# Kernel tuning notes

Measured on AMD Instinct MI355X. Metric: run time of the kernel, lower is better.

The kernel has to match this reference:

```python
import jax, jax.numpy as jnp
import numpy as np

HEADS = 16
DV = 64  # value_out_channel
DK = 64  # key_out_channel == query_out_channel
DQ = 64  # query_out_channel


def setup_inputs() -> dict:
    key = jax.random.key(0)
    ks = jax.random.split(key, 7)
    B, Skv, Ekv = 4, 2048, 1024
    Sq, Eq = 2048, 1024
    x = jax.random.normal(ks[0], (B, Skv, Ekv), dtype=jnp.float32)
    y = jax.random.normal(ks[1], (B, Sq, Eq), dtype=jnp.float32)
    # Linear weights stored as [in, out] for x @ W; no bias on qkv (bias=False)
    Wv = jax.random.normal(ks[2], (Ekv, HEADS * DV), dtype=jnp.float32) * (Ekv ** -0.5)
    Wk = jax.random.normal(ks[3], (Ekv, HEADS * DK), dtype=jnp.float32) * (Ekv ** -0.5)
    Wq = jax.random.normal(ks[4], (Eq, HEADS * DQ), dtype=jnp.float32) * (Eq ** -0.5)
    Wu = jax.random.normal(ks[5], (HEADS * DV, DQ), dtype=jnp.float32) * ((HEADS * DV) ** -0.5)
    bu = jax.random.normal(ks[6], (DQ,), dtype=jnp.float32) * 0.01
    return {"x": x, "y": y, "Wv": Wv, "Wk": Wk, "Wq": Wq, "Wu": Wu, "bu": bu}


def reference(x, y, Wv, Wk, Wq, Wu, bu):
    B, Skv, Ekv = x.shape
    _, Sq, Eq = y.shape
    v = (x @ Wv).reshape(B, Skv, HEADS, DV)
    k = (x @ Wk).reshape(B, Skv, HEADS, DK)
    q = (y @ Wq).reshape(B, Sq, HEADS, DQ)
    # scaling uses INPUT embedding dims, as in the source
    q = q * (Eq ** -0.25)
    k = k * (Ekv ** -0.25)
    dot = jnp.einsum("bqhd,bkhd->bhqk", q, k)  # [B, H, Sq, Skv]
    attn = jax.nn.softmax(dot, axis=-1)
    out = jnp.einsum("bhqk,bkhd->bqhd", attn, v).reshape(B, Sq, HEADS * DV)
    return out @ Wu + bu
```

## Files before the change

kernel.cpp:

```cpp
#include <hip/hip_runtime.h>
#include <hip/hip_bf16.h>
#include <stdint.h>

typedef short s16x8 __attribute__((ext_vector_type(8)));
typedef float f32x4 __attribute__((ext_vector_type(4)));

#define MFMA16(a, b, c) __builtin_amdgcn_mfma_f32_16x16x32_bf16((a), (b), (c), 0, 0, 0)

__device__ __forceinline__ void gld16(const __bf16* g, __bf16* l) {
  __builtin_amdgcn_global_load_lds(
      (const __attribute__((address_space(1))) unsigned int*)g,
      (__attribute__((address_space(3))) unsigned int*)l, 16, 0, 0);
}

__device__ __forceinline__ float fast_exp2(float x) {
#if __has_builtin(__builtin_amdgcn_exp2f)
  return __builtin_amdgcn_exp2f(x);
#else
  float r;
  asm("v_exp_f32 %0, %1" : "=v"(r) : "v"(x));
  return r;
#endif
}

__global__ void probe_kernel(const unsigned short* __restrict__ x, int* __restrict__ flag) {
  int cnt = 0;
  for (int i = threadIdx.x; i < 1024; i += 64) {
    unsigned bits = ((unsigned)x[2 * i]) << 16;
    float f = __uint_as_float(bits);
    float a = fabsf(f);
    if (f == f && a >= 1e-4f && a <= 1e4f) cnt++;
  }
#pragma unroll
  for (int off = 32; off; off >>= 1) cnt += __shfl_down(cnt, off);
  if (threadIdx.x == 0) *flag = (cnt >= 512) ? 1 : 0;
}

__global__ void cvt2_kernel(const void* __restrict__ ia, const void* __restrict__ ib,
                            __bf16* __restrict__ oa, __bf16* __restrict__ ob,
                            int nvec, const int* __restrict__ flag) {
  const bool isbf = (*flag != 0);
  int i = blockIdx.x * blockDim.x + threadIdx.x;
  int stride = gridDim.x * blockDim.x;
  for (; i < 2 * nvec; i += stride) {
    int v = (i < nvec) ? i : i - nvec;
    const void* in = (i < nvec) ? ia : ib;
    __bf16* out = (i < nvec) ? oa : ob;
    if (isbf) {
      *(uint4*)&out[v * 8] = *(const uint4*)&((const __bf16*)in)[v * 8];
    } else {
      float4 a = *(const float4*)&((const float*)in)[v * 8];
      float4 b = *(const float4*)&((const float*)in)[v * 8 + 4];
      union { __bf16 h[8]; uint4 u; } pk;
      pk.h[0] = (__bf16)a.x; pk.h[1] = (__bf16)a.y; pk.h[2] = (__bf16)a.z; pk.h[3] = (__bf16)a.w;
      pk.h[4] = (__bf16)b.x; pk.h[5] = (__bf16)b.y; pk.h[6] = (__bf16)b.z; pk.h[7] = (__bf16)b.w;
      *(uint4*)&out[v * 8] = pk.u;
    }
  }
}

__global__ void tr3_kernel(const void* __restrict__ w0, const void* __restrict__ w1,
                           const void* __restrict__ w2, const void* __restrict__ w3,
                           __bf16* __restrict__ outbase, __bf16* __restrict__ out3,
                           const int* __restrict__ flag) {
  const bool isbf = (*flag != 0);
  const int z = blockIdx.z;
  if (z == 3 && blockIdx.x >= 2) return;
  const void* in = (z == 0) ? w0 : (z == 1) ? w1 : (z == 2) ? w2 : w3;
  __bf16* out = (z == 3) ? out3 : outbase + (size_t)z * 1024 * 1024;
  const int N = (z == 3) ? 64 : 1024;
  __shared__ float tile[32][33];
  int tx = threadIdx.x & 31, ty = threadIdx.x >> 5;
  int n0 = blockIdx.x * 32, k0 = blockIdx.y * 32;
#pragma unroll
  for (int i = 0; i < 32; i += 8) {
    size_t idx = (size_t)(k0 + ty + i) * N + (n0 + tx);
    tile[ty + i][tx] = isbf ? (float)((const __bf16*)in)[idx] : ((const float*)in)[idx];
  }
  __syncthreads();
#pragma unroll
  for (int i = 0; i < 32; i += 8)
    out[(size_t)(n0 + ty + i) * 1024 + (k0 + tx)] = (__bf16)tile[tx][ty + i];
}

template <int BM, int BN, bool BIAS, bool C_WS>
__global__ void __launch_bounds__(256)
gemm_lds(const __bf16* __restrict__ A, const __bf16* __restrict__ Bt,
         void* __restrict__ Cv, const void* __restrict__ biasv,
         int M, int N, int K, float scale, const int* __restrict__ flag) {
  constexpr int BK = 32;
  __shared__ __attribute__((aligned(16))) __bf16 As[BM * BK];
  __shared__ __attribute__((aligned(16))) __bf16 Bs[BN * BK];
  constexpr int WM = BM / 2, WN = BN / 2;
  constexpr int MT = WM / 16, NT = WN / 16;

  const bool raw_bf = (*flag != 0);
  const int tid = threadIdx.x;
  const int wid = tid >> 6, lane = tid & 63;
  const int quad = lane >> 4, l16 = lane & 15;
  const int wm = (wid >> 1) * WM, wn = (wid & 1) * WN;
  const size_t m0 = (size_t)blockIdx.x * BM;
  const size_t n0 = (size_t)blockIdx.y * BN;

  f32x4 acc[MT][NT];
#pragma unroll
  for (int i = 0; i < MT; ++i)
#pragma unroll
    for (int j = 0; j < NT; ++j) acc[i][j] = (f32x4){0.f, 0.f, 0.f, 0.f};

  for (int k0 = 0; k0 < K; k0 += BK) {
#pragma unroll
    for (int i = 0; i < (BM * 4) / 256; ++i) {
      int s = i * 256 + tid, r = s >> 2, c = (s & 3) * 8;
      gld16(&A[(m0 + r) * K + k0 + c], &As[(i * 256 + (tid & 192)) * 8]);
    }
#pragma unroll
    for (int i = 0; i < (BN * 4) / 256; ++i) {
      int s = i * 256 + tid, r = s >> 2, c = (s & 3) * 8;
      gld16(&Bt[(n0 + r) * K + k0 + c], &Bs[(i * 256 + (tid & 192)) * 8]);
    }
    __syncthreads();

    s16x8 af[MT], bf[NT];
#pragma unroll
    for (int mt = 0; mt < MT; ++mt)
      af[mt] = *(const s16x8*)&As[(wm + mt * 16 + l16) * BK + quad * 8];
#pragma unroll
    for (int nt = 0; nt < NT; ++nt)
      bf[nt] = *(const s16x8*)&Bs[(wn + nt * 16 + l16) * BK + quad * 8];
#pragma unroll
    for (int mt = 0; mt < MT; ++mt)
#pragma unroll
      for (int nt = 0; nt < NT; ++nt)
        acc[mt][nt] = MFMA16(af[mt], bf[nt], acc[mt][nt]);
    __syncthreads();
  }

#pragma unroll
  for (int mt = 0; mt < MT; ++mt)
#pragma unroll
    for (int nt = 0; nt < NT; ++nt)
#pragma unroll
      for (int r = 0; r < 4; ++r) {
        size_t row = m0 + wm + mt * 16 + quad * 4 + r;
        size_t col = n0 + wn + nt * 16 + l16;
        float v = acc[mt][nt][r] * scale;
        if (BIAS)
          v += raw_bf ? (float)((const __bf16*)biasv)[col] : ((const float*)biasv)[col];
        if (C_WS || raw_bf) ((__bf16*)Cv)[row * N + col] = (__bf16)v;
        else                ((float*)Cv)[row * N + col] = v;
      }
}

__global__ void __launch_bounds__(256)
gemm_qkv(const __bf16* __restrict__ xb, const __bf16* __restrict__ yb,
         const __bf16* __restrict__ Wt,
         __bf16* __restrict__ qb, __bf16* __restrict__ kb, __bf16* __restrict__ vbT,
         float scq, float sck) {
  constexpr int BM = 128, BN = 128, BK = 32, K = 1024;
  __shared__ __attribute__((aligned(16))) __bf16 As[BM * BK];
  __shared__ __attribute__((aligned(16))) __bf16 Bs[BN * BK];

  const int tid = threadIdx.x;
  const int wid = tid >> 6, lane = tid & 63;
  const int quad = lane >> 4, l16 = lane & 15;
  const int wm = (wid >> 1) * 64, wn = (wid & 1) * 64;

  const int id = blockIdx.x;
  const int jj = id >> 3;
  const int ny = (id & 7) * 3 + (jj % 3);
  const int mb = jj / 3;
  const size_t m0 = (size_t)mb * BM;
  const size_t n0 = (size_t)ny * BN;
  const __bf16* A = (ny < 8) ? yb : xb;

  f32x4 acc[4][4];
#pragma unroll
  for (int i = 0; i < 4; ++i)
#pragma unroll
    for (int j = 0; j < 4; ++j) acc[i][j] = (f32x4){0.f, 0.f, 0.f, 0.f};

  for (int k0 = 0; k0 < K; k0 += BK) {
#pragma unroll
    for (int i = 0; i < 2; ++i) {
      int s = i * 256 + tid, r = s >> 2, c = (s & 3) * 8;
      gld16(&A[(m0 + r) * K + k0 + c], &As[(i * 256 + (tid & 192)) * 8]);
    }
#pragma unroll
    for (int i = 0; i < 2; ++i) {
      int s = i * 256 + tid, r = s >> 2, c = (s & 3) * 8;
      gld16(&Wt[(n0 + r) * K + k0 + c], &Bs[(i * 256 + (tid & 192)) * 8]);
    }
    __syncthreads();

    s16x8 af[4], bf[4];
#pragma unroll
    for (int mt = 0; mt < 4; ++mt)
      af[mt] = *(const s16x8*)&As[(wm + mt * 16 + l16) * BK + quad * 8];
#pragma unroll
    for (int nt = 0; nt < 4; ++nt)
      bf[nt] = *(const s16x8*)&Bs[(wn + nt * 16 + l16) * BK + quad * 8];
#pragma unroll
    for (int mt = 0; mt < 4; ++mt)
#pragma unroll
      for (int nt = 0; nt < 4; ++nt)
        acc[mt][nt] = MFMA16(af[mt], bf[nt], acc[mt][nt]);
    __syncthreads();
  }

  if (ny < 16) {
    const float s = (ny < 8) ? scq : sck;
    __bf16* C = (ny < 8) ? qb : kb;
    const int nl0 = (ny < 8) ? (int)n0 : (int)n0 - 1024;
#pragma unroll
    for (int mt = 0; mt < 4; ++mt)
#pragma unroll
      for (int nt = 0; nt < 4; ++nt)
#pragma unroll
        for (int r = 0; r < 4; ++r) {
          size_t row = m0 + wm + mt * 16 + quad * 4 + r;
          size_t col = (size_t)(nl0 + wn + nt * 16 + l16);
          C[row * 1024 + col] = (__bf16)(acc[mt][nt][r] * s);
        }
  } else {
    constexpr int LBS = 144;
    __bf16* bufA = As;
    __bf16* bufB = Bs;
    __bf16* mybuf = (wid & 1) ? bufB : bufA;
    const int colbase = (int)n0 - 2048;
    const int b = (int)(m0 >> 11);
    const int sq0 = (int)(m0 & 2047);
#pragma unroll
    for (int c = 0; c < 4; ++c) {
#pragma unroll
      for (int mt = 0; mt < 4; ++mt) {
        union { __bf16 h[4]; uint2 u; } pk;
#pragma unroll
        for (int r = 0; r < 4; ++r) pk.h[r] = (__bf16)acc[mt][c][r];
        *(uint2*)&mybuf[l16 * LBS + wm + mt * 16 + quad * 4] = pk.u;
      }
      __syncthreads();
      {
        const int p = tid >> 7;
        const __bf16* rb = p ? bufB : bufA;
        const int d16 = (tid >> 3) & 15;
        const int sc = tid & 7;
        const int colg = colbase + p * 64 + c * 16 + d16;
        const int hh = colg >> 6, dd = colg & 63;
        const size_t rowb = ((size_t)b * 16 + hh) * 64 + dd;
        uint4 v0 = *(const uint4*)&rb[d16 * LBS + sc * 16];
        uint4 v1 = *(const uint4*)&rb[d16 * LBS + sc * 16 + 8];
        *(uint4*)&vbT[rowb * 2048 + sq0 + sc * 16] = v0;
        *(uint4*)&vbT[rowb * 2048 + sq0 + sc * 16 + 8] = v1;
      }
      __syncthreads();
    }
  }
}

__global__ void __launch_bounds__(256)
gemm_out(const __bf16* __restrict__ A, const __bf16* __restrict__ Bt,
         void* __restrict__ Cv, const void* __restrict__ biasv,
         const int* __restrict__ flag) {
  constexpr int BK = 64, K = 1024, N = 64;
  __shared__ __attribute__((aligned(16))) __bf16 As[32 * BK];
  __shared__ __attribute__((aligned(16))) __bf16 Bs[64 * BK];

  const bool raw_bf = (*flag != 0);
  const int tid = threadIdx.x;
  const int wid = tid >> 6, lane = tid & 63;
  const int quad = lane >> 4, l16 = lane & 15;
  const int wm = (wid >> 1) * 16, wn = (wid & 1) * 32;
  const size_t m0 = (size_t)blockIdx.x * 32;

  f32x4 acc[2];
  acc[0] = (f32x4){0.f, 0.f, 0.f, 0.f};
  acc[1] = (f32x4){0.f, 0.f, 0.f, 0.f};

  for (int k0 = 0; k0 < K; k0 += BK) {
    {
      int r = tid >> 3, c = (tid & 7) * 8;
      gld16(&A[(m0 + r) * K + k0 + c], &As[(tid & 192) * 8]);
    }
#pragma unroll
    for (int i = 0; i < 2; ++i) {
      int s = i * 256 + tid, r = s >> 3, c = (s & 7) * 8;
      gld16(&Bt[r * K + k0 + c], &Bs[(i * 256 + (tid & 192)) * 8]);
    }
    __syncthreads();

#pragma unroll
    for (int kc = 0; kc < 2; ++kc) {
      s16x8 af = *(const s16x8*)&As[(wm + l16) * BK + kc * 32 + quad * 8];
#pragma unroll
      for (int nt = 0; nt < 2; ++nt) {
        s16x8 bf = *(const s16x8*)&Bs[(wn + nt * 16 + l16) * BK + kc * 32 + quad * 8];
        acc[nt] = MFMA16(af, bf, acc[nt]);
      }
    }
    __syncthreads();
  }

#pragma unroll
  for (int nt = 0; nt < 2; ++nt)
#pragma unroll
    for (int r = 0; r < 4; ++r) {
      size_t row = m0 + wm + quad * 4 + r;
      size_t col = (size_t)(wn + nt * 16 + l16);
      float v = acc[nt][r];
      v += raw_bf ? (float)((const __bf16*)biasv)[col] : ((const float*)biasv)[col];
      if (raw_bf) ((__bf16*)Cv)[row * N + col] = (__bf16)v;
      else        ((float*)Cv)[row * N + col] = v;
    }
}

template <int BM, int BN, bool BIAS, bool A_WS, bool C_WS>
__global__ void __launch_bounds__(256)
gemm_bt(const void* __restrict__ Av, const __bf16* __restrict__ Bt,
        void* __restrict__ Cv, const void* __restrict__ biasv,
        int M, int N, int K, float scale, const int* __restrict__ flag) {
  constexpr int BK = 32;
  constexpr int LDT = BK + 8;
  __shared__ __attribute__((aligned(16))) __bf16 As[BM][LDT];
  __shared__ __attribute__((aligned(16))) __bf16 Bs[BN][LDT];
  constexpr int WM = BM / 2, WN = BN / 2;
  constexpr int MT = WM / 16, NT = WN / 16;

  const bool raw_bf = (*flag != 0);
  const bool a_bf = A_WS ? true : raw_bf;

  const int tid = threadIdx.x;
  const int wid = tid >> 6, lane = tid & 63;
  const int quad = lane >> 4, l16 = lane & 15;
  const int wm = (wid >> 1) * WM, wn = (wid & 1) * WN;
  const size_t m0 = (size_t)blockIdx.x * BM;
  const size_t n0 = (size_t)blockIdx.y * BN;

  f32x4 acc[MT][NT];
#pragma unroll
  for (int i = 0; i < MT; ++i)
#pragma unroll
    for (int j = 0; j < NT; ++j) acc[i][j] = (f32x4){0.f, 0.f, 0.f, 0.f};

  for (int k0 = 0; k0 < K; k0 += BK) {
    if (a_bf) {
      const __bf16* A = (const __bf16*)Av;
#pragma unroll
      for (int i = 0; i < (BM * 4) / 256; ++i) {
        int s = i * 256 + tid, r = s >> 2, c = (s & 3) * 8;
        *(uint4*)&As[r][c] = *(const uint4*)&A[(m0 + r) * K + k0 + c];
      }
    } else {
      const float* A = (const float*)Av;
#pragma unroll
      for (int i = 0; i < (BM * 8) / 256; ++i) {
        int s = i * 256 + tid, r = s >> 3, c = (s & 7) * 4;
        float4 t = *(const float4*)&A[(m0 + r) * K + k0 + c];
        union { __bf16 h[4]; uint2 u; } cv;
        cv.h[0] = (__bf16)t.x; cv.h[1] = (__bf16)t.y;
        cv.h[2] = (__bf16)t.z; cv.h[3] = (__bf16)t.w;
        *(uint2*)&As[r][c] = cv.u;
      }
    }
#pragma unroll
    for (int i = 0; i < (BN * 4) / 256; ++i) {
      int s = i * 256 + tid, r = s >> 2, c = (s & 3) * 8;
      *(uint4*)&Bs[r][c] = *(const uint4*)&Bt[(n0 + r) * K + k0 + c];
    }
    __syncthreads();

    s16x8 af[MT], bf[NT];
#pragma unroll
    for (int mt = 0; mt < MT; ++mt)
      af[mt] = *(const s16x8*)&As[wm + mt * 16 + l16][quad * 8];
#pragma unroll
    for (int nt = 0; nt < NT; ++nt)
      bf[nt] = *(const s16x8*)&Bs[wn + nt * 16 + l16][quad * 8];
#pragma unroll
    for (int mt = 0; mt < MT; ++mt)
#pragma unroll
      for (int nt = 0; nt < NT; ++nt)
        acc[mt][nt] = MFMA16(af[mt], bf[nt], acc[mt][nt]);
    __syncthreads();
  }

#pragma unroll
  for (int mt = 0; mt < MT; ++mt)
#pragma unroll
    for (int nt = 0; nt < NT; ++nt)
#pragma unroll
      for (int r = 0; r < 4; ++r) {
        size_t row = m0 + wm + mt * 16 + quad * 4 + r;
        size_t col = n0 + wn + nt * 16 + l16;
        float v = acc[mt][nt][r] * scale;
        if (BIAS)
          v += raw_bf ? (float)((const __bf16*)biasv)[col] : ((const float*)biasv)[col];
        if (C_WS || raw_bf) ((__bf16*)Cv)[row * N + col] = (__bf16)v;
        else                ((float*)Cv)[row * N + col] = v;
      }
}

__global__ void __launch_bounds__(256, 4)
attn5_kernel(const __bf16* __restrict__ qg, const __bf16* __restrict__ kg,
             const __bf16* __restrict__ vtg, __bf16* __restrict__ og) {
  constexpr int SKV = 2048, QT = 128, KT = 64, SS = 1024, VS = 2048;
  __shared__ __attribute__((aligned(16))) __bf16 QP[QT * 64];
  __shared__ __attribute__((aligned(16))) __bf16 Ks[KT * 64];
  __shared__ __attribute__((aligned(16))) __bf16 Vt[2][64 * KT];

  const int tid = threadIdx.x;
  const int wid = tid >> 6, lane = tid & 63;
  const int quad = lane >> 4, l16 = lane & 15;

  const int id = blockIdx.x;
  const int j = id >> 3;
  const int bh = (id & 7) * 8 + (j & 7);
  const int b = bh >> 4, h = bh & 15;
  const int q0 = (j >> 3) * QT;

  const __bf16* qb = qg + (size_t)b * 2048 * SS + h * 64;
  const __bf16* kb = kg + (size_t)b * 2048 * SS + h * 64;
  const __bf16* vtb = vtg + (size_t)bh * 64 * VS;
  __bf16* ob = og + (size_t)b * 2048 * SS + h * 64;

#pragma unroll
  for (int i = 0; i < 4; ++i) {
    int s = i * 256 + tid, r = s >> 3, slot = s & 7, c = slot ^ (r & 7);
    gld16(&qb[(size_t)(q0 + r) * SS + c * 8], &QP[(i * 256 + (tid & 192)) * 8]);
  }
  __syncthreads();

  s16x8 qf[2][2];
#pragma unroll
  for (int nt = 0; nt < 2; ++nt)
#pragma unroll
    for (int kc = 0; kc < 2; ++kc) {
      int row = wid * 32 + nt * 16 + l16;
      qf[nt][kc] = *(const s16x8*)&QP[row * 64 + (((quad + kc * 4) ^ (row & 7)) * 8)];
    }
  __syncthreads();

  int koff[4][2];
  int pwoff[2][4];
  int proff[2][2];
  int voff[2][4];
#pragma unroll
  for (int mtk = 0; mtk < 4; ++mtk)
#pragma unroll
    for (int kc = 0; kc < 2; ++kc) {
      int row = mtk * 16 + l16;
      koff[mtk][kc] = row * 64 + (((quad + kc * 4) ^ (row & 7)) * 8);
    }
#pragma unroll
  for (int ntq = 0; ntq < 2; ++ntq) {
    int row = wid * 32 + ntq * 16 + l16;
#pragma unroll
    for (int mtk = 0; mtk < 4; ++mtk)
      pwoff[ntq][mtk] = row * 64 + (((2 * mtk + (quad >> 1)) ^ (row & 7)) * 8) + (quad & 1) * 4;
#pragma unroll
    for (int kc = 0; kc < 2; ++kc)
      proff[ntq][kc] = row * 64 + (((4 * kc + quad) ^ (row & 7)) * 8);
  }
#pragma unroll
  for (int kc = 0; kc < 2; ++kc)
#pragma unroll
    for (int ntd = 0; ntd < 4; ++ntd) {
      int d = ntd * 16 + l16;
      voff[kc][ntd] = d * 64 + (((kc * 4 + quad) ^ (d & 7)) * 8);
    }

  float lsum[2] = {0.f, 0.f};
  f32x4 oacc[2][4];
#pragma unroll
  for (int mt = 0; mt < 2; ++mt)
#pragma unroll
    for (int nt = 0; nt < 4; ++nt) oacc[mt][nt] = (f32x4){0.f, 0.f, 0.f, 0.f};

#pragma unroll
  for (int i = 0; i < 2; ++i) {
    int s = i * 256 + tid, r = s >> 3, slot = s & 7, c = slot ^ (r & 7);
    gld16(&vtb[(size_t)r * VS + c * 8], &Vt[0][(i * 256 + (tid & 192)) * 8]);
  }
#pragma unroll
  for (int i = 0; i < 2; ++i) {
    int s = i * 256 + tid, r = s >> 3, slot = s & 7, c = slot ^ (r & 7);
    gld16(&kb[(size_t)r * SS + c * 8], &Ks[(i * 256 + (tid & 192)) * 8]);
  }

  for (int kv = 0; kv < SKV; kv += KT) {
    const int cur = (kv >> 6) & 1;
    asm volatile("s_waitcnt vmcnt(0)" ::: "memory");
    __builtin_amdgcn_s_barrier();
    asm volatile("" ::: "memory");

    if (kv + KT < SKV) {
#pragma unroll
      for (int i = 0; i < 2; ++i) {
        int s = i * 256 + tid, r = s >> 3, slot = s & 7, c = slot ^ (r & 7);
        gld16(&vtb[(size_t)r * VS + (kv + KT) + c * 8],
              &Vt[cur ^ 1][(i * 256 + (tid & 192)) * 8]);
      }
    }

#pragma unroll
    for (int mtk = 0; mtk < 4; ++mtk) {
      s16x8 kfa[2];
#pragma unroll
      for (int kc = 0; kc < 2; ++kc)
        kfa[kc] = *(const s16x8*)&Ks[koff[mtk][kc]];
#pragma unroll
      for (int ntq = 0; ntq < 2; ++ntq) {
        f32x4 z = (f32x4){0.f, 0.f, 0.f, 0.f};
        __builtin_amdgcn_s_setprio(1);
        z = MFMA16(kfa[0], qf[ntq][0], z);
        z = MFMA16(kfa[1], qf[ntq][1], z);
        __builtin_amdgcn_s_setprio(0);
        union { __bf16 hh[4]; uint2 u; } pk;
        float p0 = fast_exp2(z[0]);
        float p1 = fast_exp2(z[1]);
        float p2 = fast_exp2(z[2]);
        float p3 = fast_exp2(z[3]);
        pk.hh[0] = (__bf16)p0; pk.hh[1] = (__bf16)p1;
        pk.hh[2] = (__bf16)p2; pk.hh[3] = (__bf16)p3;
        lsum[ntq] += (p0 + p1) + (p2 + p3);
        *(uint2*)&QP[pwoff[ntq][mtk]] = pk.u;
      }
    }

    asm volatile("" ::: "memory");
    __builtin_amdgcn_s_barrier();
    asm volatile("" ::: "memory");

    if (kv + KT < SKV) {
#pragma unroll
      for (int i = 0; i < 2; ++i) {
        int s = i * 256 + tid, r = s >> 3, slot = s & 7, c = slot ^ (r & 7);
        gld16(&kb[(size_t)(kv + KT + r) * SS + c * 8], &Ks[(i * 256 + (tid & 192)) * 8]);
      }
    }

#pragma unroll
    for (int kc = 0; kc < 2; ++kc) {
      s16x8 pf[2], vf[4];
#pragma unroll
      for (int mt2 = 0; mt2 < 2; ++mt2)
        pf[mt2] = *(const s16x8*)&QP[proff[mt2][kc]];
#pragma unroll
      for (int ntd = 0; ntd < 4; ++ntd)
        vf[ntd] = *(const s16x8*)&Vt[cur][voff[kc][ntd]];
      __builtin_amdgcn_s_setprio(1);
#pragma unroll
      for (int mt2 = 0; mt2 < 2; ++mt2)
#pragma unroll
        for (int ntd = 0; ntd < 4; ++ntd)
          oacc[mt2][ntd] = MFMA16(pf[mt2], vf[ntd], oacc[mt2][ntd]);
      __builtin_amdgcn_s_setprio(0);
    }
  }

#pragma unroll
  for (int nt = 0; nt < 2; ++nt) {
    lsum[nt] += __shfl_xor(lsum[nt], 16);
    lsum[nt] += __shfl_xor(lsum[nt], 32);
  }
#pragma unroll
  for (int mt2 = 0; mt2 < 2; ++mt2)
#pragma unroll
    for (int r = 0; r < 4; ++r) {
      float l = __shfl(lsum[mt2], quad * 4 + r);
      float linv = 1.0f / l;
      int row = q0 + wid * 32 + mt2 * 16 + quad * 4 + r;
#pragma unroll
      for (int ntd = 0; ntd < 4; ++ntd)
        ob[(size_t)row * SS + ntd * 16 + l16] = (__bf16)(oacc[mt2][ntd][r] * linv);
    }
}

__global__ void __launch_bounds__(256)
attn_kernel(const __bf16* __restrict__ qg, const __bf16* __restrict__ kg,
            const __bf16* __restrict__ vg, __bf16* __restrict__ og) {
  constexpr int D = 64, SKV = 2048, QT = 128, KT = 64, SS = 1024;
  constexpr int LDP = 72, LDV = 72;
  __shared__ __attribute__((aligned(16))) __bf16 QP[QT * LDP];
  __shared__ __attribute__((aligned(16))) __bf16 Ks[KT * D];
  __shared__ __attribute__((aligned(16))) __bf16 Vts[D * LDV];

  const int tid = threadIdx.x;
  const int wid = tid >> 6, lane = tid & 63;
  const int quad = lane >> 4, l16 = lane & 15;
  const int b = blockIdx.y >> 4, h = blockIdx.y & 15;
  const int q0 = blockIdx.x * QT;

  const __bf16* qb = qg + (size_t)b * 2048 * SS + h * D;
  const __bf16* kb = kg + (size_t)b * 2048 * SS + h * D;
  const __bf16* vb = vg + (size_t)b * 2048 * SS + h * D;
  __bf16* ob = og + (size_t)b * 2048 * SS + h * D;

#pragma unroll
  for (int i = 0; i < 4; ++i) {
    int s = i * 256 + tid, r = s >> 3, slot = s & 7, c = slot ^ (r & 7);
    gld16(&qb[(size_t)(q0 + r) * SS + c * 8], &QP[(i * 256 + (tid & 192)) * 8]);
  }
  __syncthreads();

  s16x8 qf[2][2];
#pragma unroll
  for (int nt = 0; nt < 2; ++nt)
#pragma unroll
    for (int kc = 0; kc < 2; ++kc) {
      int row = wid * 32 + nt * 16 + l16;
      qf[nt][kc] = *(const s16x8*)&QP[row * 64 + (((quad + kc * 4) ^ (row & 7)) * 8)];
    }
  __syncthreads();

  float lsum[2] = {0.f, 0.f};
  f32x4 oacc[2][4];
#pragma unroll
  for (int mt = 0; mt < 2; ++mt)
#pragma unroll
    for (int nt = 0; nt < 4; ++nt) oacc[mt][nt] = (f32x4){0.f, 0.f, 0.f, 0.f};

  for (int kv = 0; kv < SKV; kv += KT) {
#pragma unroll
    for (int i = 0; i < 2; ++i) {
      int s = i * 256 + tid, r = s >> 3, slot = s & 7, c = slot ^ (r & 7);
      gld16(&kb[(size_t)(kv + r) * SS + c * 8], &Ks[(i * 256 + (tid & 192)) * 8]);
    }
#pragma unroll
    for (int i = 0; i < 2; ++i) {
      int s = i * 256 + tid, r = s >> 3, mc = s & 7;
      uint4 t = *(const uint4*)&vb[(size_t)(kv + r) * SS + mc * 8];
      const __bf16* tp = (const __bf16*)&t;
      int colbase = r ^ (mc << 3);
#pragma unroll
      for (int jj = 0; jj < 8; ++jj) Vts[(mc * 8 + jj) * LDV + colbase] = tp[jj];
    }
    __syncthreads();

#pragma unroll
    for (int mtk = 0; mtk < 4; ++mtk) {
      s16x8 kfa[2];
#pragma unroll
      for (int kc = 0; kc < 2; ++kc) {
        int row = mtk * 16 + l16;
        kfa[kc] = *(const s16x8*)&Ks[row * 64 + (((quad + kc * 4) ^ (row & 7)) * 8)];
      }
#pragma unroll
      for (int ntq = 0; ntq < 2; ++ntq) {
        f32x4 z = (f32x4){0.f, 0.f, 0.f, 0.f};
        z = MFMA16(kfa[0], qf[ntq][0], z);
        z = MFMA16(kfa[1], qf[ntq][1], z);
        union { __bf16 hh[4]; uint2 u; } pk;
        float ps = 0.f;
#pragma unroll
        for (int r = 0; r < 4; ++r) {
          float p = __builtin_exp2f(fminf(z[r], 80.f));
          ps += p;
          pk.hh[r] = (__bf16)p;
        }
        lsum[ntq] += ps;
        int row = wid * 32 + ntq * 16 + l16;
        *(uint2*)&QP[row * LDP + mtk * 16 + quad * 4] = pk.u;
      }
    }

#pragma unroll
    for (int kc = 0; kc < 2; ++kc) {
      s16x8 pf[2], vf[4];
#pragma unroll
      for (int mt2 = 0; mt2 < 2; ++mt2)
        pf[mt2] = *(const s16x8*)&QP[(wid * 32 + mt2 * 16 + l16) * LDP + kc * 32 + quad * 8];
#pragma unroll
      for (int ntd = 0; ntd < 4; ++ntd) {
        int d = ntd * 16 + l16;
        int col0 = (kc * 32 + quad * 8) ^ ((((d >> 3) & 7)) << 3);
        vf[ntd] = *(const s16x8*)&Vts[d * LDV + col0];
      }
#pragma unroll
      for (int mt2 = 0; mt2 < 2; ++mt2)
#pragma unroll
        for (int ntd = 0; ntd < 4; ++ntd)
          oacc[mt2][ntd] = MFMA16(pf[mt2], vf[ntd], oacc[mt2][ntd]);
    }
    __syncthreads();
  }

#pragma unroll
  for (int nt = 0; nt < 2; ++nt) {
    lsum[nt] += __shfl_xor(lsum[nt], 16);
    lsum[nt] += __shfl_xor(lsum[nt], 32);
  }
#pragma unroll
  for (int mt2 = 0; mt2 < 2; ++mt2)
#pragma unroll
    for (int r = 0; r < 4; ++r) {
      float l = __shfl(lsum[mt2], quad * 4 + r);
      float linv = 1.0f / l;
      int row = q0 + wid * 32 + mt2 * 16 + quad * 4 + r;
#pragma unroll
      for (int ntd = 0; ntd < 4; ++ntd)
        ob[(size_t)row * SS + ntd * 16 + l16] = (__bf16)(oacc[mt2][ntd][r] * linv);
    }
}

extern "C" void kernel_launch(void* const* d_in, const int* in_sizes, int n_in,
                              void* d_out, int out_size, void* d_ws, size_t ws_size,
                              hipStream_t stream) {
  const void* x  = d_in[0];
  const void* y  = d_in[1];
  const void* Wv = d_in[2];
  const void* Wk = d_in[3];
  const void* Wq = d_in[4];
  const void* Wu = d_in[5];
  const void* bu = d_in[6];

  const float sc  = 0.17677669529663687f;
  const float scq = 0.17677669529663687f * 1.4426950408889634f;

  constexpr size_t NTOK = (size_t)8192 * 1024;
  constexpr size_t TB = NTOK * 2;

  char* p = (char*)d_ws;
  int* flag = (int*)p; p += 256;
  __bf16* qb = (__bf16*)p; p += TB;
  __bf16* kb = (__bf16*)p; p += TB;
  __bf16* vb = (__bf16*)p; p += TB;
  __bf16* WuT = (__bf16*)p; p += (size_t)64 * 1024 * 2;

  probe_kernel<<<1, 64, 0, stream>>>((const unsigned short*)x, flag);

  const size_t fast_need = 256 + 3 * TB + (size_t)64 * 1024 * 2 + 2 * TB + 3 * (size_t)1024 * 1024 * 2;
  if (ws_size >= fast_need) {
    __bf16* xb = (__bf16*)p; p += TB;
    __bf16* yb = (__bf16*)p; p += TB;
    __bf16* WqkvT = (__bf16*)p;
    __bf16* vbT = vb;
    __bf16* ob  = xb;

    cvt2_kernel<<<2048, 256, 0, stream>>>(x, y, xb, yb, (int)(NTOK / 8), flag);
    tr3_kernel<<<dim3(32, 32, 4), 256, 0, stream>>>(Wq, Wk, Wv, Wu, WqkvT, WuT, flag);

    gemm_qkv<<<dim3(1536), 256, 0, stream>>>(xb, yb, WqkvT, qb, kb, vbT, scq, sc);

    attn5_kernel<<<dim3(1024), 256, 0, stream>>>(qb, kb, vbT, ob);

    gemm_out<<<dim3(256), 256, 0, stream>>>(ob, WuT, d_out, bu, flag);
  } else {
    __bf16* region = (__bf16*)p;
    __bf16* WqT = region;
    __bf16* WkT = region + (size_t)1024 * 1024;
    __bf16* WvT = region + (size_t)2 * 1024 * 1024;
    __bf16* ob  = region;

    tr3_kernel<<<dim3(32, 32, 4), 256, 0, stream>>>(Wq, Wk, Wv, Wu, WqT, WuT, flag);

    gemm_bt<128, 128, false, false, true><<<dim3(64, 8), 256, 0, stream>>>(
        y, WqT, qb, nullptr, 8192, 1024, 1024, scq, flag);
    gemm_bt<128, 128, false, false, true><<<dim3(64, 8), 256, 0, stream>>>(
        x, WkT, kb, nullptr, 8192, 1024, 1024, sc, flag);
    gemm_bt<128, 128, false, false, true><<<dim3(64, 8), 256, 0, stream>>>(
        x, WvT, vb, nullptr, 8192, 1024, 1024, 1.0f, flag);

    attn_kernel<<<dim3(16, 64), 256, 0, stream>>>(qb, kb, vb, ob);

    gemm_bt<128, 64, true, true, false><<<dim3(64, 1), 256, 0, stream>>>(
        ob, WuT, d_out, bu, 8192, 64, 1024, 1.0f, flag);
  }
}
```

Baseline: 280.1 us.

## Fuse probe, convert and weight transpose into one pre-kernel; single-buffer V in attention

Merges the dtype probe, the x/y bf16 conversion and the weight transposes into one launch, with each block redoing the probe locally. gemm_out also probes locally instead of reading a global flag. This removes two kernel launches and the serial dependency on the tiny probe kernel. Separately, the attention kernel drops V double buffering: V is now loaded into a single LDS buffer each iteration with an extra vmcnt wait. That frees LDS but exposes V load latency.

```diff
diff --git a/kernel.cpp b/kernel.cpp
--- a/kernel.cpp
+++ b/kernel.cpp
@@ -23,39 +23,78 @@
 #endif
 }
 
-__global__ void probe_kernel(const unsigned short* __restrict__ x, int* __restrict__ flag) {
+__device__ __forceinline__ int probe_cnt_wave(const unsigned short* xs, int lane) {
   int cnt = 0;
-  for (int i = threadIdx.x; i < 1024; i += 64) {
-    unsigned bits = ((unsigned)x[2 * i]) << 16;
+  for (int i = lane; i < 1024; i += 64) {
+    unsigned bits = ((unsigned)xs[2 * i]) << 16;
     float f = __uint_as_float(bits);
     float a = fabsf(f);
     if (f == f && a >= 1e-4f && a <= 1e4f) cnt++;
   }
 #pragma unroll
   for (int off = 32; off; off >>= 1) cnt += __shfl_down(cnt, off);
+  return cnt;
+}
+
+__global__ void probe_kernel(const unsigned short* __restrict__ x, int* __restrict__ flag) {
+  int cnt = probe_cnt_wave(x, threadIdx.x & 63);
   if (threadIdx.x == 0) *flag = (cnt >= 512) ? 1 : 0;
 }
 
-__global__ void cvt2_kernel(const void* __restrict__ ia, const void* __restrict__ ib,
-                            __bf16* __restrict__ oa, __bf16* __restrict__ ob,
-                            int nvec, const int* __restrict__ flag) {
-  const bool isbf = (*flag != 0);
-  int i = blockIdx.x * blockDim.x + threadIdx.x;
-  int stride = gridDim.x * blockDim.x;
-  for (; i < 2 * nvec; i += stride) {
-    int v = (i < nvec) ? i : i - nvec;
-    const void* in = (i < nvec) ? ia : ib;
-    __bf16* out = (i < nvec) ? oa : ob;
-    if (isbf) {
-      *(uint4*)&out[v * 8] = *(const uint4*)&((const __bf16*)in)[v * 8];
-    } else {
-      float4 a = *(const float4*)&((const float*)in)[v * 8];
-      float4 b = *(const float4*)&((const float*)in)[v * 8 + 4];
-      union { __bf16 h[8]; uint4 u; } pk;
-      pk.h[0] = (__bf16)a.x; pk.h[1] = (__bf16)a.y; pk.h[2] = (__bf16)a.z; pk.h[3] = (__bf16)a.w;
-      pk.h[4] = (__bf16)b.x; pk.h[5] = (__bf16)b.y; pk.h[6] = (__bf16)b.z; pk.h[7] = (__bf16)b.w;
-      *(uint4*)&out[v * 8] = pk.u;
-    }
+__global__ void __launch_bounds__(256)
+pre_kernel(const void* __restrict__ x, const void* __restrict__ y,
+           const void* __restrict__ w0, const void* __restrict__ w1,
+           const void* __restrict__ w2, const void* __restrict__ w3,
+           __bf16* __restrict__ xb, __bf16* __restrict__ yb,
+           __bf16* __restrict__ wqkvT, __bf16* __restrict__ wuT) {
+  __shared__ int sflag;
+  __shared__ float tile[32][33];
+  if (threadIdx.x < 64) {
+    int cnt = probe_cnt_wave((const unsigned short*)x, threadIdx.x);
+    if (threadIdx.x == 0) sflag = (cnt >= 512) ? 1 : 0;
+  }
+  __syncthreads();
+  const bool isbf = (sflag != 0);
+
+  const int bid = blockIdx.x;
+  if (bid < 2048) {
+    constexpr int NV = (int)((size_t)8192 * 1024 / 8);
+    int i = bid * 256 + threadIdx.x;
+    const int stride = 2048 * 256;
+    for (; i < 2 * NV; i += stride) {
+      int v = (i < NV) ? i : i - NV;
+      const void* in = (i < NV) ? x : y;
+      __bf16* out = (i < NV) ? xb : yb;
+      if (isbf) {
+        *(uint4*)&out[v * 8] = *(const uint4*)&((const __bf16*)in)[v * 8];
+      } else {
+        float4 a = *(const float4*)&((const float*)in)[v * 8];
+        float4 b = *(const float4*)&((const float*)in)[v * 8 + 4];
+        union { __bf16 h[8]; uint4 u; } pk;
+        pk.h[0] = (__bf16)a.x; pk.h[1] = (__bf16)a.y; pk.h[2] = (__bf16)a.z; pk.h[3] = (__bf16)a.w;
+        pk.h[4] = (__bf16)b.x; pk.h[5] = (__bf16)b.y; pk.h[6] = (__bf16)b.z; pk.h[7] = (__bf16)b.w;
+        *(uint4*)&out[v * 8] = pk.u;
+      }
+    }
+  } else {
+    int t = bid - 2048;
+    int z, bx, by;
+    if (t < 3072) { z = t >> 10; int xy = t & 1023; bx = xy & 31; by = xy >> 5; }
+    else          { z = 3; int u = t - 3072; bx = u & 1; by = u >> 1; }
+    const void* in = (z == 0) ? w0 : (z == 1) ? w1 : (z == 2) ? w2 : w3;
+    __bf16* out = (z == 3) ? wuT : wqkvT + (size_t)z * 1024 * 1024;
+    const int N = (z == 3) ? 64 : 1024;
+    int tx = threadIdx.x & 31, ty = threadIdx.x >> 5;
+    int n0 = bx * 32, k0 = by * 32;
+#pragma unroll
+    for (int i = 0; i < 32; i += 8) {
+      size_t idx = (size_t)(k0 + ty + i) * N + (n0 + tx);
+      tile[ty + i][tx] = isbf ? (float)((const __bf16*)in)[idx] : ((const float*)in)[idx];
+    }
+    __syncthreads();
+#pragma unroll
+    for (int i = 0; i < 32; i += 8)
+      out[(size_t)(n0 + ty + i) * 1024 + (k0 + tx)] = (__bf16)tile[tx][ty + i];
   }
 }
 
@@ -83,75 +122,6 @@
     out[(size_t)(n0 + ty + i) * 1024 + (k0 + tx)] = (__bf16)tile[tx][ty + i];
 }
 
-template <int BM, int BN, bool BIAS, bool C_WS>
-__global__ void __launch_bounds__(256)
-gemm_lds(const __bf16* __restrict__ A, const __bf16* __restrict__ Bt,
-         void* __restrict__ Cv, const void* __restrict__ biasv,
-         int M, int N, int K, float scale, const int* __restrict__ flag) {
-  constexpr int BK = 32;
-  __shared__ __attribute__((aligned(16))) __bf16 As[BM * BK];
-  __shared__ __attribute__((aligned(16))) __bf16 Bs[BN * BK];
-  constexpr int WM = BM / 2, WN = BN / 2;
-  constexpr int MT = WM / 16, NT = WN / 16;
-
-  const bool raw_bf = (*flag != 0);
-  const int tid = threadIdx.x;
-  const int wid = tid >> 6, lane = tid & 63;
-  const int quad = lane >> 4, l16 = lane & 15;
-  const int wm = (wid >> 1) * WM, wn = (wid & 1) * WN;
-  const size_t m0 = (size_t)blockIdx.x * BM;
-  const size_t n0 = (size_t)blockIdx.y * BN;
-
-  f32x4 acc[MT][NT];
-#pragma unroll
-  for (int i = 0; i < MT; ++i)
-#pragma unroll
-    for (int j = 0; j < NT; ++j) acc[i][j] = (f32x4){0.f, 0.f, 0.f, 0.f};
-
-  for (int k0 = 0; k0 < K; k0 += BK) {
-#pragma unroll
-    for (int i = 0; i < (BM * 4) / 256; ++i) {
-      int s = i * 256 + tid, r = s >> 2, c = (s & 3) * 8;
-      gld16(&A[(m0 + r) * K + k0 + c], &As[(i * 256 + (tid & 192)) * 8]);
-    }
-#pragma unroll
-    for (int i = 0; i < (BN * 4) / 256; ++i) {
-      int s = i * 256 + tid, r = s >> 2, c = (s & 3) * 8;
-      gld16(&Bt[(n0 + r) * K + k0 + c], &Bs[(i * 256 + (tid & 192)) * 8]);
-    }
-    __syncthreads();
-
-    s16x8 af[MT], bf[NT];
-#pragma unroll
-    for (int mt = 0; mt < MT; ++mt)
-      af[mt] = *(const s16x8*)&As[(wm + mt * 16 + l16) * BK + quad * 8];
-#pragma unroll
-    for (int nt = 0; nt < NT; ++nt)
-      bf[nt] = *(const s16x8*)&Bs[(wn + nt * 16 + l16) * BK + quad * 8];
-#pragma unroll
-    for (int mt = 0; mt < MT; ++mt)
-#pragma unroll
-      for (int nt = 0; nt < NT; ++nt)
-        acc[mt][nt] = MFMA16(af[mt], bf[nt], acc[mt][nt]);
-    __syncthreads();
-  }
-
-#pragma unroll
-  for (int mt = 0; mt < MT; ++mt)
-#pragma unroll
-    for (int nt = 0; nt < NT; ++nt)
-#pragma unroll
-      for (int r = 0; r < 4; ++r) {
-        size_t row = m0 + wm + mt * 16 + quad * 4 + r;
-        size_t col = n0 + wn + nt * 16 + l16;
-        float v = acc[mt][nt][r] * scale;
-        if (BIAS)
-          v += raw_bf ? (float)((const __bf16*)biasv)[col] : ((const float*)biasv)[col];
-        if (C_WS || raw_bf) ((__bf16*)Cv)[row * N + col] = (__bf16)v;
-        else                ((float*)Cv)[row * N + col] = v;
-      }
-}
-
 __global__ void __launch_bounds__(256)
 gemm_qkv(const __bf16* __restrict__ xb, const __bf16* __restrict__ yb,
          const __bf16* __restrict__ Wt,
@@ -261,13 +231,18 @@
 __global__ void __launch_bounds__(256)
 gemm_out(const __bf16* __restrict__ A, const __bf16* __restrict__ Bt,
          void* __restrict__ Cv, const void* __restrict__ biasv,
-         const int* __restrict__ flag) {
+         const unsigned short* __restrict__ xprobe) {
   constexpr int BK = 64, K = 1024, N = 64;
   __shared__ __attribute__((aligned(16))) __bf16 As[32 * BK];
   __shared__ __attribute__((aligned(16))) __bf16 Bs[64 * BK];
-
-  const bool raw_bf = (*flag != 0);
+  __shared__ int sflag;
+
   const int tid = threadIdx.x;
+  if (tid < 64) {
+    int cnt = probe_cnt_wave(xprobe, tid);
+    if (tid == 0) sflag = (cnt >= 512) ? 1 : 0;
+  }
+
   const int wid = tid >> 6, lane = tid & 63;
   const int quad = lane >> 4, l16 = lane & 15;
   const int wm = (wid >> 1) * 16, wn = (wid & 1) * 32;
@@ -301,6 +276,7 @@
     __syncthreads();
   }
 
+  const bool raw_bf = (sflag != 0);
 #pragma unroll
   for (int nt = 0; nt < 2; ++nt)
 #pragma unroll
@@ -406,7 +382,7 @@
   constexpr int SKV = 2048, QT = 128, KT = 64, SS = 1024, VS = 2048;
   __shared__ __attribute__((aligned(16))) __bf16 QP[QT * 64];
   __shared__ __attribute__((aligned(16))) __bf16 Ks[KT * 64];
-  __shared__ __attribute__((aligned(16))) __bf16 Vt[2][64 * KT];
+  __shared__ __attribute__((aligned(16))) __bf16 Vt[64 * KT];
 
   const int tid = threadIdx.x;
   const int wid = tid >> 6, lane = tid & 63;
@@ -479,27 +455,17 @@
 #pragma unroll
   for (int i = 0; i < 2; ++i) {
     int s = i * 256 + tid, r = s >> 3, slot = s & 7, c = slot ^ (r & 7);
-    gld16(&vtb[(size_t)r * VS + c * 8], &Vt[0][(i * 256 + (tid & 192)) * 8]);
-  }
-#pragma unroll
-  for (int i = 0; i < 2; ++i) {
-    int s = i * 256 + tid, r = s >> 3, slot = s & 7, c = slot ^ (r & 7);
     gld16(&kb[(size_t)r * SS + c * 8], &Ks[(i * 256 + (tid & 192)) * 8]);
   }
 
   for (int kv = 0; kv < SKV; kv += KT) {
-    const int cur = (kv >> 6) & 1;
     asm volatile("s_waitcnt vmcnt(0)" ::: "memory");
     __builtin_amdgcn_s_barrier();
-    asm volatile("" ::: "memory");
-
-    if (kv + KT < SKV) {
-#pragma unroll
-      for (int i = 0; i < 2; ++i) {
-        int s = i * 256 + tid, r = s >> 3, slot = s & 7, c = slot ^ (r & 7);
-        gld16(&vtb[(size_t)r * VS + (kv + KT) + c * 8],
-              &Vt[cur ^ 1][(i * 256 + (tid & 192)) * 8]);
-      }
+
+#pragma unroll
+    for (int i = 0; i < 2; ++i) {
+      int s = i * 256 + tid, r = s >> 3, slot = s & 7, c = slot ^ (r & 7);
+      gld16(&vtb[(size_t)r * VS + kv + c * 8], &Vt[(i * 256 + (tid & 192)) * 8]);
     }
 
 #pragma unroll
@@ -527,9 +493,8 @@
       }
     }
 
-    asm volatile("" ::: "memory");
+    asm volatile("s_waitcnt vmcnt(0)" ::: "memory");
     __builtin_amdgcn_s_barrier();
-    asm volatile("" ::: "memory");
 
     if (kv + KT < SKV) {
 #pragma unroll
@@ -547,7 +512,7 @@
         pf[mt2] = *(const s16x8*)&QP[proff[mt2][kc]];
 #pragma unroll
       for (int ntd = 0; ntd < 4; ++ntd)
-        vf[ntd] = *(const s16x8*)&Vt[cur][voff[kc][ntd]];
+        vf[ntd] = *(const s16x8*)&Vt[voff[kc][ntd]];
       __builtin_amdgcn_s_setprio(1);
 #pragma unroll
       for (int mt2 = 0; mt2 < 2; ++mt2)
@@ -727,8 +692,6 @@
   __bf16* vb = (__bf16*)p; p += TB;
   __bf16* WuT = (__bf16*)p; p += (size_t)64 * 1024 * 2;
 
-  probe_kernel<<<1, 64, 0, stream>>>((const unsigned short*)x, flag);
-
   const size_t fast_need = 256 + 3 * TB + (size_t)64 * 1024 * 2 + 2 * TB + 3 * (size_t)1024 * 1024 * 2;
   if (ws_size >= fast_need) {
     __bf16* xb = (__bf16*)p; p += TB;
@@ -737,14 +700,13 @@
     __bf16* vbT = vb;
     __bf16* ob  = xb;
 
-    cvt2_kernel<<<2048, 256, 0, stream>>>(x, y, xb, yb, (int)(NTOK / 8), flag);
-    tr3_kernel<<<dim3(32, 32, 4), 256, 0, stream>>>(Wq, Wk, Wv, Wu, WqkvT, WuT, flag);
+    pre_kernel<<<dim3(5184), 256, 0, stream>>>(x, y, Wq, Wk, Wv, Wu, xb, yb, WqkvT, WuT);
 
     gemm_qkv<<<dim3(1536), 256, 0, stream>>>(xb, yb, WqkvT, qb, kb, vbT, scq, sc);
 
     attn5_kernel<<<dim3(1024), 256, 0, stream>>>(qb, kb, vbT, ob);
 
-    gemm_out<<<dim3(256), 256, 0, stream>>>(ob, WuT, d_out, bu, flag);
+    gemm_out<<<dim3(256), 256, 0, stream>>>(ob, WuT, d_out, bu, (const unsigned short*)x);
   } else {
     __bf16* region = (__bf16*)p;
     __bf16* WqT = region;
@@ -752,6 +714,7 @@
     __bf16* WvT = region + (size_t)2 * 1024 * 1024;
     __bf16* ob  = region;
 
+    probe_kernel<<<1, 64, 0, stream>>>((const unsigned short*)x, flag);
     tr3_kernel<<<dim3(32, 32, 4), 256, 0, stream>>>(Wq, Wk, Wv, Wu, WqT, WuT, flag);
 
     gemm_bt<128, 128, false, false, true><<<dim3(64, 8), 256, 0, stream>>>(
```

After: 276.5 us. Within noise of the previous version (-1.3%).
